# Kernel optimization log

Hardware: AMD Instinct MI355X
Metric: run time of the kernel (lower is better)

The kernel has to match this reference:

```python
import jax, jax.numpy as jnp
import numpy as np

SLICES = [(12, 1), (13, 1)]  # (input_width, hidden_size=1) per slice


def _lstm_last_hidden(xs, W_ih, W_hh, b):
    """Run a standard (PyTorch gate order i,f,g,o) LSTM over time, return last h.
    xs: [T, B, in]; W_ih: [4*H, in]; W_hh: [4*H, H]; b: [4*H] (b_ih + b_hh).
    Returns h_T: [B, H].
    """
    B = xs.shape[1]
    H = W_hh.shape[1]
    h0 = jnp.zeros((B, H), xs.dtype)
    c0 = jnp.zeros((B, H), xs.dtype)

    def step(carry, xt):
        h, c = carry
        gates = xt @ W_ih.T + h @ W_hh.T + b  # [B, 4H]
        i, f, g, o = jnp.split(gates, 4, axis=-1)
        i = jax.nn.sigmoid(i)
        f = jax.nn.sigmoid(f)
        g = jnp.tanh(g)
        o = jax.nn.sigmoid(o)
        c = f * c + i * g
        h = o * jnp.tanh(c)
        return (h, c), None

    (hT, _), _ = jax.lax.scan(step, (h0, c0), xs)
    return hT


def setup_inputs() -> dict:
    key = jax.random.key(0)
    ks = jax.random.split(key, 9)
    B, T, F = 4096, 512, 25
    nb_out = 1
    s = 0.1
    x = jax.random.normal(ks[0], (B, T, F), dtype=jnp.float32)
    # slice-1 LSTM (input 12, hidden 1)
    W_ih1 = jax.random.normal(ks[1], (4, 12), dtype=jnp.float32) * s
    W_hh1 = jax.random.normal(ks[2], (4, 1), dtype=jnp.float32) * s
    b1 = jax.random.normal(ks[3], (4,), dtype=jnp.float32) * s
    # slice-2 LSTM (input 13, hidden 1)
    W_ih2 = jax.random.normal(ks[4], (4, 13), dtype=jnp.float32) * s
    W_hh2 = jax.random.normal(ks[5], (4, 1), dtype=jnp.float32) * s
    b2 = jax.random.normal(ks[6], (4,), dtype=jnp.float32) * s
    # output head Linear(2, nb_out)
    W_out = jax.random.normal(ks[7], (nb_out, 2), dtype=jnp.float32) * s
    b_out = jax.random.normal(ks[8], (nb_out,), dtype=jnp.float32) * s
    return {"x": x, "W_ih1": W_ih1, "W_hh1": W_hh1, "b1": b1,
            "W_ih2": W_ih2, "W_hh2": W_hh2, "b2": b2,
            "W_out": W_out, "b_out": b_out}


def reference(x, W_ih1, W_hh1, b1, W_ih2, W_hh2, b2, W_out, b_out):
    # x: [B, T, 25] -> time-major [T, B, 25]
    xs = jnp.transpose(x, (1, 0, 2))
    h1 = _lstm_last_hidden(xs[..., :12], W_ih1, W_hh1, b1)   # [B, 1]
    h2 = _lstm_last_hidden(xs[..., 12:], W_ih2, W_hh2, b2)   # [B, 1]
    h = jnp.concatenate([h1, h2], axis=-1)                   # [B, 2] == lstm_out[:, -1, :]
    out = h @ W_out.T + b_out                                # [B, nb_out]
    return jax.nn.sigmoid(out)
```

## Files before the change

kernel.cpp:

```cpp
#include <hip/hip_runtime.h>
#include <stdint.h>


#define T_STEPS 512
#define F_IN    25
#define TC      16
#define NTILES  (T_STEPS / TC)
#define CH      4
#define XROW    520
#define ZROW    136
#define XBUF    (CH * XROW)
#define ZBUF    (CH * ZROW)
#define LOG2E   1.44269504088896340736f

typedef const __attribute__((address_space(1))) void* as1_cvp;
typedef __attribute__((address_space(3)))       void* as3_vp;

__device__ __forceinline__ void gll16(const float* gsrc, const float* ldst) {
  __builtin_amdgcn_global_load_lds((as1_cvp)(uintptr_t)gsrc,
                                   (as3_vp)(uint32_t)(uintptr_t)ldst, 16, 0, 0);
}

__device__ __forceinline__ float sigm(float v) {
  return __builtin_amdgcn_rcpf(1.0f + __builtin_amdgcn_exp2f(v * (-LOG2E)));
}
__device__ __forceinline__ float tanh_(float v) {
  return fmaf(2.0f, __builtin_amdgcn_rcpf(1.0f + __builtin_amdgcn_exp2f(v * (-2.0f * LOG2E))), -1.0f);
}

__device__ __forceinline__ void prefetch_tile(const float* __restrict__ x, int b0, int tile,
                                              float* xbuf, int lane) {
  const float* base = x + (size_t)b0 * (T_STEPS * F_IN) + tile * (TC * F_IN);
  const int i1 = lane * 4;
  int i2 = 256 + lane * 4;
  if (i2 > 396) i2 = 396;
#pragma unroll
  for (int cc = 0; cc < CH; ++cc) {
    const float* g0 = base + cc * (T_STEPS * F_IN);
    gll16(g0 + i1, xbuf + cc * XROW);
    gll16(g0 + i2, xbuf + cc * XROW + 256);
  }
}

__device__ __forceinline__ void gemv_tile(const float* __restrict__ xbuf, float* __restrict__ zbuf,
                                          int cg, int lt, int xoff, int zoff,
                                          const float* __restrict__ w, const float* __restrict__ zb) {
#pragma unroll
  for (int p = 0; p < 2; ++p) {
    const int tl = p * 8 + lt;
    const float* xr = xbuf + cg * XROW + tl * F_IN + xoff;
    float z0 = zb[0], z1 = zb[1], z2 = zb[2], z3 = zb[3];
#pragma unroll
    for (int f = 0; f < 13; ++f) {
      const float xv = xr[f];
      z0 = fmaf(w[0 * 13 + f], xv, z0);
      z1 = fmaf(w[1 * 13 + f], xv, z1);
      z2 = fmaf(w[2 * 13 + f], xv, z2);
      z3 = fmaf(w[3 * 13 + f], xv, z3);
    }
    *(float4*)(zbuf + cg * ZROW + tl * 8 + zoff) = make_float4(z0, z1, z2, z3);
  }
}

__device__ __forceinline__ void scan_tile(const float* __restrict__ zbuf, int cs, int zoff,
                                          const float* __restrict__ whh, float& hv, float& cv) {
#pragma unroll
  for (int t = 0; t < TC; ++t) {
    const float4 z4 = *(const float4*)(zbuf + cs * ZROW + t * 8 + zoff);
    const float pi = fmaf(hv, whh[0], z4.x);
    const float pf = fmaf(hv, whh[1], z4.y);
    const float pg = fmaf(hv, whh[2], z4.z);
    const float po = fmaf(hv, whh[3], z4.w);
    const float ai = sigm(pi);
    const float af = sigm(pf);
    const float ag = tanh_(pg);
    const float ao = sigm(po);
    cv = fmaf(af, cv, ai * ag);
    hv = ao * tanh_(cv);
  }
}

__global__ void __launch_bounds__(64, 1)
lstm2_fused(const float* __restrict__ x,
            const float* __restrict__ Wih1, const float* __restrict__ Whh1, const float* __restrict__ b1,
            const float* __restrict__ Wih2, const float* __restrict__ Whh2, const float* __restrict__ b2,
            const float* __restrict__ Wout, const float* __restrict__ bout,
            float* __restrict__ out)
{
  __shared__ __align__(16) float xs[3 * XBUF];
  __shared__ __align__(16) float zs[2 * ZBUF];

  const int lane = threadIdx.x;
  const int cg   = lane >> 4;
  const int hg   = (lane >> 3) & 1;
  const int lt   = lane & 7;
  const int xoff = hg * 12;
  const int zofg = hg * 4;
  const int cs   = lane & 3;
  const int hs   = (lane >> 2) & 1;
  const int zofs = hs * 4;
  const int b0   = blockIdx.x * CH;

  float w[52], zb[4], whh[4];
#pragma unroll
  for (int j = 0; j < 4; ++j) {
#pragma unroll
    for (int f = 0; f < 13; ++f) {
      const float wa = (f < 12) ? Wih1[j * 12 + f] : 0.0f;
      const float wb = Wih2[j * 13 + f];
      w[j * 13 + f] = hg ? wb : wa;
    }
    zb[j]  = hg ? b2[j]   : b1[j];
    whh[j] = hs ? Whh2[j] : Whh1[j];
  }

  float hv = 0.0f, cv = 0.0f;

  prefetch_tile(x, b0, 0, xs + 0 * XBUF, lane);
  prefetch_tile(x, b0, 1, xs + 1 * XBUF, lane);
  prefetch_tile(x, b0, 2, xs + 2 * XBUF, lane);
  asm volatile("s_waitcnt vmcnt(16)" ::: "memory");
  gemv_tile(xs, zs, cg, lt, xoff, zofg, w, zb);
  asm volatile("s_waitcnt lgkmcnt(0)" ::: "memory");

  int pb = 0;
  int rb = 1;
  for (int k = 0; k < NTILES - 1; ++k) {
    asm volatile("s_waitcnt vmcnt(8)" ::: "memory");
    int tn = k + 3;
    if (tn > NTILES - 1) tn = NTILES - 1;
    prefetch_tile(x, b0, tn, xs + pb * XBUF, lane);
    pb = (pb == 2) ? 0 : pb + 1;
    const float* zrd = zs + (k & 1) * ZBUF;
    float*       zwr = zs + ((k + 1) & 1) * ZBUF;
    const float* xrd = xs + rb * XBUF;
    rb = (rb == 2) ? 0 : rb + 1;
    scan_tile(zrd, cs, zofs, whh, hv, cv);
    gemv_tile(xrd, zwr, cg, lt, xoff, zofg, w, zb);
    asm volatile("s_waitcnt lgkmcnt(0)" ::: "memory");
  }
  scan_tile(zs + ZBUF, cs, zofs, whh, hv, cv);
  asm volatile("s_waitcnt vmcnt(0)" ::: "memory");

  const float h1 = __shfl(hv, (lane & 3), 64);
  const float h2 = __shfl(hv, (lane & 3) + 4, 64);
  if (lane < 4) {
    out[b0 + lane] = sigm(fmaf(Wout[0], h1, fmaf(Wout[1], h2, bout[0])));
  }
}

extern "C" void kernel_launch(void* const* d_in, const int* in_sizes, int n_in,
                              void* d_out, int out_size, void* d_ws, size_t ws_size,
                              hipStream_t stream) {
  const float* x    = (const float*)d_in[0];
  const float* Wih1 = (const float*)d_in[1];
  const float* Whh1 = (const float*)d_in[2];
  const float* b1   = (const float*)d_in[3];
  const float* Wih2 = (const float*)d_in[4];
  const float* Whh2 = (const float*)d_in[5];
  const float* b2   = (const float*)d_in[6];
  const float* Wout = (const float*)d_in[7];
  const float* bout = (const float*)d_in[8];
  float* out = (float*)d_out;

  const int B = in_sizes[0] / (T_STEPS * F_IN);
  dim3 grid(B / CH), block(64);
  hipLaunchKernelGGL(lstm2_fused, grid, block, 0, stream,
                     x, Wih1, Whh1, b1, Wih2, Whh2, b2, Wout, bout, out);
}
```

Baseline: 307.1 us.

## Specialize waves into loader/GEMV producers and a dedicated recurrent scan wave

Each block now covers 16 batch chains with 192 threads. Two waves prefetch x tiles into LDS and compute the input projections, while a third wave runs only the serial LSTM recurrence on the projections from the previous tile, with a block barrier per tile. The aim is to take the GEMV and load waits off the latency-bound scan path and overlap the two across waves. In exchange there are fewer blocks, one scan wave per CU with half its lanes idle, and a barrier on every tile.

```diff
diff --git a/kernel.cpp b/kernel.cpp
--- a/kernel.cpp
+++ b/kernel.cpp
@@ -6,11 +6,12 @@
 #define F_IN    25
 #define TC      16
 #define NTILES  (T_STEPS / TC)
-#define CH      4
+#define CH      16
+#define CPW     8
 #define XROW    520
-#define ZROW    136
 #define XBUF    (CH * XROW)
-#define ZBUF    (CH * ZROW)
+#define ZROWP   132
+#define ZBUF    (TC * ZROWP)
 #define LOG2E   1.44269504088896340736f
 
 typedef const __attribute__((address_space(1))) void* as1_cvp;
@@ -28,27 +29,32 @@
   return fmaf(2.0f, __builtin_amdgcn_rcpf(1.0f + __builtin_amdgcn_exp2f(v * (-2.0f * LOG2E))), -1.0f);
 }
 
-__device__ __forceinline__ void prefetch_tile(const float* __restrict__ x, int b0, int tile,
-                                              float* xbuf, int lane) {
-  const float* base = x + (size_t)b0 * (T_STEPS * F_IN) + tile * (TC * F_IN);
+__device__ __forceinline__ void prefetch_tile(const float* __restrict__ x, int b0, int wid,
+                                              int tile, float* xbuf, int lane) {
+  const float* base = x + (size_t)(b0 + wid * CPW) * (T_STEPS * F_IN) + tile * (TC * F_IN);
+  float* l0 = xbuf + (wid * CPW) * XROW;
   const int i1 = lane * 4;
   int i2 = 256 + lane * 4;
   if (i2 > 396) i2 = 396;
 #pragma unroll
-  for (int cc = 0; cc < CH; ++cc) {
+  for (int cc = 0; cc < CPW; ++cc) {
     const float* g0 = base + cc * (T_STEPS * F_IN);
-    gll16(g0 + i1, xbuf + cc * XROW);
-    gll16(g0 + i2, xbuf + cc * XROW + 256);
+    gll16(g0 + i1, l0 + cc * XROW);
+    gll16(g0 + i2, l0 + cc * XROW + 256);
   }
 }
 
-__device__ __forceinline__ void gemv_tile(const float* __restrict__ xbuf, float* __restrict__ zbuf,
-                                          int cg, int lt, int xoff, int zoff,
+__device__ __forceinline__ void gemv_tile(const float* __restrict__ xbuf, float* __restrict__ zwr,
+                                          int lane, int wid,
                                           const float* __restrict__ w, const float* __restrict__ zb) {
+  const int t    = lane & 15;
+  const int h    = (lane >> 4) & 1;
+  const int chl  = lane >> 5;
+  const int xoff = h * 12;
 #pragma unroll
-  for (int p = 0; p < 2; ++p) {
-    const int tl = p * 8 + lt;
-    const float* xr = xbuf + cg * XROW + tl * F_IN + xoff;
+  for (int p = 0; p < 4; ++p) {
+    const int cg = wid * CPW + p * 2 + chl;
+    const float* xr = xbuf + cg * XROW + t * F_IN + xoff;
     float z0 = zb[0], z1 = zb[1], z2 = zb[2], z3 = zb[3];
 #pragma unroll
     for (int f = 0; f < 13; ++f) {
@@ -58,15 +64,16 @@
       z2 = fmaf(w[2 * 13 + f], xv, z2);
       z3 = fmaf(w[3 * 13 + f], xv, z3);
     }
-    *(float4*)(zbuf + cg * ZROW + tl * 8 + zoff) = make_float4(z0, z1, z2, z3);
+    const int rec = 2 * cg + h;
+    *(float4*)(zwr + t * ZROWP + rec * 4) = make_float4(z0, z1, z2, z3);
   }
 }
 
-__device__ __forceinline__ void scan_tile(const float* __restrict__ zbuf, int cs, int zoff,
+__device__ __forceinline__ void scan_tile(const float* __restrict__ zrd, int rec,
                                           const float* __restrict__ whh, float& hv, float& cv) {
 #pragma unroll
   for (int t = 0; t < TC; ++t) {
-    const float4 z4 = *(const float4*)(zbuf + cs * ZROW + t * 8 + zoff);
+    const float4 z4 = *(const float4*)(zrd + t * ZROWP + rec * 4);
     const float pi = fmaf(hv, whh[0], z4.x);
     const float pf = fmaf(hv, whh[1], z4.y);
     const float pg = fmaf(hv, whh[2], z4.z);
@@ -80,7 +87,7 @@
   }
 }
 
-__global__ void __launch_bounds__(64, 1)
+__global__ void __launch_bounds__(192, 1)
 lstm2_fused(const float* __restrict__ x,
             const float* __restrict__ Wih1, const float* __restrict__ Whh1, const float* __restrict__ b1,
             const float* __restrict__ Wih2, const float* __restrict__ Whh2, const float* __restrict__ b2,
@@ -90,17 +97,12 @@
   __shared__ __align__(16) float xs[3 * XBUF];
   __shared__ __align__(16) float zs[2 * ZBUF];
 
-  const int lane = threadIdx.x;
-  const int cg   = lane >> 4;
-  const int hg   = (lane >> 3) & 1;
-  const int lt   = lane & 7;
-  const int xoff = hg * 12;
-  const int zofg = hg * 4;
-  const int cs   = lane & 3;
-  const int hs   = (lane >> 2) & 1;
-  const int zofs = hs * 4;
+  const int lane = threadIdx.x & 63;
+  const int wid  = threadIdx.x >> 6;
   const int b0   = blockIdx.x * CH;
 
+  const int hg = (lane >> 4) & 1;
+  const int hs = lane & 1;
   float w[52], zb[4], whh[4];
 #pragma unroll
   for (int j = 0; j < 4; ++j) {
@@ -115,37 +117,41 @@
   }
 
   float hv = 0.0f, cv = 0.0f;
+  const int rec = lane & 31;
 
-  prefetch_tile(x, b0, 0, xs + 0 * XBUF, lane);
-  prefetch_tile(x, b0, 1, xs + 1 * XBUF, lane);
-  prefetch_tile(x, b0, 2, xs + 2 * XBUF, lane);
-  asm volatile("s_waitcnt vmcnt(16)" ::: "memory");
-  gemv_tile(xs, zs, cg, lt, xoff, zofg, w, zb);
-  asm volatile("s_waitcnt lgkmcnt(0)" ::: "memory");
-
-  int pb = 0;
-  int rb = 1;
-  for (int k = 0; k < NTILES - 1; ++k) {
-    asm volatile("s_waitcnt vmcnt(8)" ::: "memory");
-    int tn = k + 3;
-    if (tn > NTILES - 1) tn = NTILES - 1;
-    prefetch_tile(x, b0, tn, xs + pb * XBUF, lane);
-    pb = (pb == 2) ? 0 : pb + 1;
-    const float* zrd = zs + (k & 1) * ZBUF;
-    float*       zwr = zs + ((k + 1) & 1) * ZBUF;
-    const float* xrd = xs + rb * XBUF;
-    rb = (rb == 2) ? 0 : rb + 1;
-    scan_tile(zrd, cs, zofs, whh, hv, cv);
-    gemv_tile(xrd, zwr, cg, lt, xoff, zofg, w, zb);
+  if (wid < 2) {
+    prefetch_tile(x, b0, wid, 0, xs + 0 * XBUF, lane);
+    prefetch_tile(x, b0, wid, 1, xs + 1 * XBUF, lane);
+    prefetch_tile(x, b0, wid, 2, xs + 2 * XBUF, lane);
+    asm volatile("s_waitcnt vmcnt(32)" ::: "memory");
+    gemv_tile(xs, zs, lane, wid, w, zb);
     asm volatile("s_waitcnt lgkmcnt(0)" ::: "memory");
   }
-  scan_tile(zs + ZBUF, cs, zofs, whh, hv, cv);
-  asm volatile("s_waitcnt vmcnt(0)" ::: "memory");
+  __builtin_amdgcn_s_barrier();
 
-  const float h1 = __shfl(hv, (lane & 3), 64);
-  const float h2 = __shfl(hv, (lane & 3) + 4, 64);
-  if (lane < 4) {
-    out[b0 + lane] = sigm(fmaf(Wout[0], h1, fmaf(Wout[1], h2, bout[0])));
+  for (int k = 0; k < NTILES - 1; ++k) {
+    if (wid < 2) {
+      if (k < NTILES - 3) {
+        asm volatile("s_waitcnt vmcnt(16)" ::: "memory");
+        prefetch_tile(x, b0, wid, k + 3, xs + (k % 3) * XBUF, lane);
+      } else {
+        asm volatile("s_waitcnt vmcnt(0)" ::: "memory");
+      }
+      gemv_tile(xs + ((k + 1) % 3) * XBUF, zs + ((k + 1) & 1) * ZBUF, lane, wid, w, zb);
+      asm volatile("s_waitcnt lgkmcnt(0)" ::: "memory");
+    } else {
+      scan_tile(zs + (k & 1) * ZBUF, rec, whh, hv, cv);
+    }
+    __builtin_amdgcn_s_barrier();
+  }
+
+  if (wid == 2) {
+    scan_tile(zs + ZBUF, rec, whh, hv, cv);
+    const float h1 = __shfl(hv, (lane & 30), 64);
+    const float h2 = __shfl(hv, (lane & 30) | 1, 64);
+    if (lane < 32 && (lane & 1) == 0) {
+      out[b0 + (lane >> 1)] = sigm(fmaf(Wout[0], h1, fmaf(Wout[1], h2, bout[0])));
+    }
   }
 }
 
@@ -164,7 +170,7 @@
   float* out = (float*)d_out;
 
   const int B = in_sizes[0] / (T_STEPS * F_IN);
-  dim3 grid(B / CH), block(64);
+  dim3 grid(B / CH), block(192);
   hipLaunchKernelGGL(lstm2_fused, grid, block, 0, stream,
                      x, Wih1, Whh1, b1, Wih2, Whh2, b2, Wout, bout, out);
 }
```

After: 304.7 us. About the same (-0.8%).
